# Kernel tuning notes

Measured on AMD Instinct MI355X. Metric: run time of the kernel, lower is better.

The kernel has to match this reference:

```python
import jax, jax.numpy as jnp
import numpy as np

STD = 0.01

def setup_inputs() -> dict:
    key = jax.random.key(0)
    k1, k2, k3 = jax.random.split(key, 3)
    B, T, D = 16, 4096, 512
    x = jax.random.normal(k1, (B, T, D), dtype=jnp.float32)
    att_W = jax.random.normal(k2, (D, D), dtype=jnp.float32) * STD
    att_v = jax.random.normal(k3, (D,), dtype=jnp.float32) * STD
    return {"x": x, "att_W": att_W, "att_v": att_v}

def reference(x, att_W, att_v):
    # additive attention scores: tanh(x @ W) @ v -> [B, T]
    y = jnp.tanh(jnp.einsum('btd,de->bte', x, att_W))
    scores = jnp.einsum('btd,d->bt', y, att_v)
    weights = jax.nn.softmax(scores, axis=-1)          # softmax over sequence
    out = jnp.einsum('bt,btd->bd', weights, x)         # weighted sum pooling
    return out.astype(jnp.float32)
```

## Files before the change

kernel.cpp:

```cpp
#include <hip/hip_runtime.h>
#include <hip/hip_bf16.h>
#include <math.h>

#define BB 16
#define TT 4096
#define DD 512
#define MM (BB*TT)

typedef __bf16 bf16x8 __attribute__((ext_vector_type(8)));
typedef float  f32x4  __attribute__((ext_vector_type(4)));

__device__ inline unsigned short f2bf(float f) {
    unsigned u = __builtin_bit_cast(unsigned, f) + 0x8000u;
    return (unsigned short)(u >> 16);
}

__device__ inline unsigned pack_bf16x2(float lo, float hi) {
    unsigned u0 = __builtin_bit_cast(unsigned, lo) + 0x8000u;
    unsigned u1 = __builtin_bit_cast(unsigned, hi) + 0x8000u;
    return __builtin_amdgcn_perm(u1, u0, 0x07060302);
}

__global__ void wt_kernel(const float* __restrict__ W, unsigned short* __restrict__ Wt) {
    int idx = blockIdx.x * 256 + threadIdx.x;
    int n = idx >> 9;
    int k = idx & 511;
    Wt[idx] = f2bf(W[k * DD + n]);
}

#define BM 128
#define BN 128
#define BK 64
#define LDA 72

__global__ __launch_bounds__(256) void scores_kernel(
        const float* __restrict__ x, const unsigned short* __restrict__ Wt,
        const float* __restrict__ v, float* __restrict__ spart) {
    __shared__ unsigned short As[BM * LDA];
    __shared__ unsigned short Bs[BN * LDA];
    __shared__ float sbuf[2][BM];

    const int tid  = threadIdx.x;
    const int m0   = blockIdx.x * BM;
    const int n0   = blockIdx.y * BN;
    const int wid  = tid >> 6;
    const int lane = tid & 63;
    const int wm   = wid >> 1;
    const int wn   = wid & 1;
    const int l15  = lane & 15;
    const int q    = lane >> 4;

    f32x4 acc[4][4];
    #pragma unroll
    for (int i = 0; i < 4; i++)
        #pragma unroll
        for (int j = 0; j < 4; j++)
            acc[i][j] = (f32x4){0.f, 0.f, 0.f, 0.f};

    for (int k0 = 0; k0 < DD; k0 += BK) {
        #pragma unroll
        for (int i = 0; i < 8; i++) {
            int idx = i * 256 + tid;
            int row = idx >> 4;
            int c4  = idx & 15;
            float4 f = *(const float4*)(x + (size_t)(m0 + row) * DD + k0 + c4 * 4);
            uint2 p;
            p.x = pack_bf16x2(f.x, f.y);
            p.y = pack_bf16x2(f.z, f.w);
            *(uint2*)(&As[row * LDA + c4 * 4]) = p;
        }
        #pragma unroll
        for (int i = 0; i < 4; i++) {
            int idx = i * 256 + tid;
            int row = idx >> 3;
            int c8  = idx & 7;
            uint4 u = *(const uint4*)(Wt + (size_t)(n0 + row) * DD + k0 + c8 * 8);
            *(uint4*)(&Bs[row * LDA + c8 * 8]) = u;
        }
        __syncthreads();

        #pragma unroll
        for (int s = 0; s < 2; s++) {
            const int ko = s * 32 + q * 8;
            bf16x8 a[4], b[4];
            #pragma unroll
            for (int mi = 0; mi < 4; mi++)
                a[mi] = *(const bf16x8*)(&As[(wm * 64 + mi * 16 + l15) * LDA + ko]);
            #pragma unroll
            for (int ni = 0; ni < 4; ni++)
                b[ni] = *(const bf16x8*)(&Bs[(wn * 64 + ni * 16 + l15) * LDA + ko]);
            #pragma unroll
            for (int mi = 0; mi < 4; mi++)
                #pragma unroll
                for (int ni = 0; ni < 4; ni++)
                    acc[mi][ni] = __builtin_amdgcn_mfma_f32_16x16x32_bf16(
                        a[mi], b[ni], acc[mi][ni], 0, 0, 0);
        }
        __syncthreads();
    }

    float vv[4];
    #pragma unroll
    for (int ni = 0; ni < 4; ni++)
        vv[ni] = v[n0 + wn * 64 + ni * 16 + l15];

    #pragma unroll
    for (int mi = 0; mi < 4; mi++) {
        #pragma unroll
        for (int r = 0; r < 4; r++) {
            float sum = 0.f;
            #pragma unroll
            for (int ni = 0; ni < 4; ni++)
                sum += tanhf(acc[mi][ni][r]) * vv[ni];
            sum += __shfl_xor(sum, 1);
            sum += __shfl_xor(sum, 2);
            sum += __shfl_xor(sum, 4);
            sum += __shfl_xor(sum, 8);
            if (l15 == 0)
                sbuf[wn][wm * 64 + mi * 16 + q * 4 + r] = sum;
        }
    }
    __syncthreads();
    if (tid < BM)
        spart[(size_t)blockIdx.y * MM + m0 + tid] = sbuf[0][tid] + sbuf[1][tid];
}

__global__ void softmax_kernel(const float* __restrict__ spart, float* __restrict__ weights) {
    const int b = blockIdx.x;
    const int tid = threadIdx.x;
    __shared__ float wred[4];

    float s[16];
    float mx = -1e30f;
    #pragma unroll
    for (int i = 0; i < 16; i++) {
        int t = b * TT + i * 256 + tid;
        float sv = spart[t] + spart[MM + t] + spart[2 * MM + t] + spart[3 * MM + t];
        s[i] = sv;
        mx = fmaxf(mx, sv);
    }
    #pragma unroll
    for (int off = 32; off; off >>= 1) mx = fmaxf(mx, __shfl_xor(mx, off));
    if ((tid & 63) == 0) wred[tid >> 6] = mx;
    __syncthreads();
    mx = fmaxf(fmaxf(wred[0], wred[1]), fmaxf(wred[2], wred[3]));
    __syncthreads();

    float sum = 0.f;
    #pragma unroll
    for (int i = 0; i < 16; i++) { s[i] = __expf(s[i] - mx); sum += s[i]; }
    #pragma unroll
    for (int off = 32; off; off >>= 1) sum += __shfl_xor(sum, off);
    if ((tid & 63) == 0) wred[tid >> 6] = sum;
    __syncthreads();
    sum = wred[0] + wred[1] + wred[2] + wred[3];

    const float inv = 1.0f / sum;
    #pragma unroll
    for (int i = 0; i < 16; i++)
        weights[b * TT + i * 256 + tid] = s[i] * inv;
}

#define TCH 128
__global__ void pool_kernel(const float* __restrict__ x, const float* __restrict__ weights,
                            float* __restrict__ out) {
    __shared__ float wsm[TCH];
    const int b  = blockIdx.y;
    const int t0 = blockIdx.x * TCH;
    const int tid = threadIdx.x;
    if (tid < TCH) wsm[tid] = weights[b * TT + t0 + tid];
    __syncthreads();

    float2 acc = {0.f, 0.f};
    const float* xp = x + ((size_t)b * TT + t0) * DD + tid * 2;
    #pragma unroll 4
    for (int t = 0; t < TCH; t++) {
        float2 xv = *(const float2*)(xp + (size_t)t * DD);
        float w = wsm[t];
        acc.x += w * xv.x;
        acc.y += w * xv.y;
    }
    atomicAdd(&out[b * DD + tid * 2],     acc.x);
    atomicAdd(&out[b * DD + tid * 2 + 1], acc.y);
}

extern "C" void kernel_launch(void* const* d_in, const int* in_sizes, int n_in,
                              void* d_out, int out_size, void* d_ws, size_t ws_size,
                              hipStream_t stream) {
    (void)in_sizes; (void)n_in; (void)out_size; (void)ws_size;
    const float* x = (const float*)d_in[0];
    const float* W = (const float*)d_in[1];
    const float* v = (const float*)d_in[2];
    float* out = (float*)d_out;

    unsigned short* Wt    = (unsigned short*)d_ws;
    float* spart          = (float*)((char*)d_ws + 512 * 1024);
    float* weights        = (float*)((char*)d_ws + 512 * 1024 + 1024 * 1024);

    hipMemsetAsync(d_out, 0, BB * DD * sizeof(float), stream);

    wt_kernel<<<DD * DD / 256, 256, 0, stream>>>(W, Wt);

    dim3 g1(MM / BM, DD / BN);
    scores_kernel<<<g1, 256, 0, stream>>>(x, Wt, v, spart);

    softmax_kernel<<<BB, 256, 0, stream>>>(spart, weights);

    pool_kernel<<<dim3(TT / TCH, BB), 256, 0, stream>>>(x, weights, out);
}
```

Baseline: 292.2 us.

## Pre-cast x to bf16 and stream tiles into LDS via global_load_lds

Adds a cast kernel that converts x to bf16 once into workspace. The scores GEMM then loads bf16 tiles of x and W straight into LDS with global_load_lds, using an XOR-swizzled layout instead of padding. The pooling kernel also reads the bf16 copy. This is meant to halve the bytes re-read across the four N-tile passes and the pooling pass, and to remove per-tile conversion work. In exchange it adds an extra full pass over x, needs a large workspace (with a fallback to the old fp32 path when the workspace is too small), and pools over rounded bf16 values of x.

```diff
diff --git a/kernel.cpp b/kernel.cpp
--- a/kernel.cpp
+++ b/kernel.cpp
@@ -19,6 +19,24 @@
     unsigned u0 = __builtin_bit_cast(unsigned, lo) + 0x8000u;
     unsigned u1 = __builtin_bit_cast(unsigned, hi) + 0x8000u;
     return __builtin_amdgcn_perm(u1, u0, 0x07060302);
+}
+
+__device__ inline void gld_lds16(const unsigned short* g, unsigned short* l) {
+    __builtin_amdgcn_global_load_lds(
+        (const __attribute__((address_space(1))) unsigned int*)(const void*)g,
+        (__attribute__((address_space(3))) unsigned int*)(void*)l, 16, 0, 0);
+}
+
+__global__ void cast_kernel(const float* __restrict__ x, unsigned short* __restrict__ xb) {
+    size_t i = (size_t)(blockIdx.x * 256 + threadIdx.x) * 8;
+    float4 f0 = *(const float4*)(x + i);
+    float4 f1 = *(const float4*)(x + i + 4);
+    uint4 o;
+    o.x = pack_bf16x2(f0.x, f0.y);
+    o.y = pack_bf16x2(f0.z, f0.w);
+    o.z = pack_bf16x2(f1.x, f1.y);
+    o.w = pack_bf16x2(f1.z, f1.w);
+    *(uint4*)(xb + i) = o;
 }
 
 __global__ void wt_kernel(const float* __restrict__ W, unsigned short* __restrict__ Wt) {
@@ -31,13 +49,12 @@
 #define BM 128
 #define BN 128
 #define BK 64
-#define LDA 72
-
-__global__ __launch_bounds__(256) void scores_kernel(
-        const float* __restrict__ x, const unsigned short* __restrict__ Wt,
+
+__global__ __launch_bounds__(256) void scores_bf16_kernel(
+        const unsigned short* __restrict__ xb, const unsigned short* __restrict__ Wt,
         const float* __restrict__ v, float* __restrict__ spart) {
-    __shared__ unsigned short As[BM * LDA];
-    __shared__ unsigned short Bs[BN * LDA];
+    __shared__ unsigned short As[BM * BK];
+    __shared__ unsigned short Bs[BN * BK];
     __shared__ float sbuf[2][BM];
 
     const int tid  = threadIdx.x;
@@ -50,6 +67,99 @@
     const int l15  = lane & 15;
     const int q    = lane >> 4;
 
+    int srow[4], scol[4];
+    #pragma unroll
+    for (int i = 0; i < 4; i++) {
+        int ci = (wid * 4 + i) * 64 + lane;
+        srow[i] = ci >> 3;
+        scol[i] = ((ci & 7) ^ (srow[i] & 7)) * 8;
+    }
+
+    f32x4 acc[4][4];
+    #pragma unroll
+    for (int i = 0; i < 4; i++)
+        #pragma unroll
+        for (int j = 0; j < 4; j++)
+            acc[i][j] = (f32x4){0.f, 0.f, 0.f, 0.f};
+
+    for (int k0 = 0; k0 < DD; k0 += BK) {
+        #pragma unroll
+        for (int i = 0; i < 4; i++) {
+            gld_lds16(xb + (size_t)(m0 + srow[i]) * DD + k0 + scol[i],
+                      &As[(wid * 4 + i) * 512]);
+            gld_lds16(Wt + (size_t)(n0 + srow[i]) * DD + k0 + scol[i],
+                      &Bs[(wid * 4 + i) * 512]);
+        }
+        __syncthreads();
+
+        #pragma unroll
+        for (int s = 0; s < 2; s++) {
+            const int c = s * 4 + q;
+            bf16x8 a[4], b[4];
+            #pragma unroll
+            for (int mi = 0; mi < 4; mi++) {
+                int R = wm * 64 + mi * 16 + l15;
+                a[mi] = *(const bf16x8*)(&As[R * BK + ((c ^ (R & 7)) * 8)]);
+            }
+            #pragma unroll
+            for (int ni = 0; ni < 4; ni++) {
+                int R = wn * 64 + ni * 16 + l15;
+                b[ni] = *(const bf16x8*)(&Bs[R * BK + ((c ^ (R & 7)) * 8)]);
+            }
+            #pragma unroll
+            for (int mi = 0; mi < 4; mi++)
+                #pragma unroll
+                for (int ni = 0; ni < 4; ni++)
+                    acc[mi][ni] = __builtin_amdgcn_mfma_f32_16x16x32_bf16(
+                        a[mi], b[ni], acc[mi][ni], 0, 0, 0);
+        }
+        __syncthreads();
+    }
+
+    float vv[4];
+    #pragma unroll
+    for (int ni = 0; ni < 4; ni++)
+        vv[ni] = v[n0 + wn * 64 + ni * 16 + l15];
+
+    #pragma unroll
+    for (int mi = 0; mi < 4; mi++) {
+        #pragma unroll
+        for (int r = 0; r < 4; r++) {
+            float sum = 0.f;
+            #pragma unroll
+            for (int ni = 0; ni < 4; ni++)
+                sum += tanhf(acc[mi][ni][r]) * vv[ni];
+            sum += __shfl_xor(sum, 1);
+            sum += __shfl_xor(sum, 2);
+            sum += __shfl_xor(sum, 4);
+            sum += __shfl_xor(sum, 8);
+            if (l15 == 0)
+                sbuf[wn][wm * 64 + mi * 16 + q * 4 + r] = sum;
+        }
+    }
+    __syncthreads();
+    if (tid < BM)
+        spart[(size_t)blockIdx.y * MM + m0 + tid] = sbuf[0][tid] + sbuf[1][tid];
+}
+
+#define LDA 72
+__global__ __launch_bounds__(256) void scores_f32_kernel(
+        const float* __restrict__ x, const unsigned short* __restrict__ Wt,
+        const float* __restrict__ v, float* __restrict__ spart) {
+    __shared__ unsigned short As[BM * LDA];
+    __shared__ unsigned short Bs[BN * LDA];
+    __shared__ float sbuf[2][BM];
+
+    const int tid  = threadIdx.x;
+    const int m0   = blockIdx.x * BM;
+    const int n0   = blockIdx.y * BN;
+    const int wid  = tid >> 6;
+    const int lane = tid & 63;
+    const int wm   = wid >> 1;
+    const int wn   = wid & 1;
+    const int l15  = lane & 15;
+    const int q    = lane >> 4;
+
     f32x4 acc[4][4];
     #pragma unroll
     for (int i = 0; i < 4; i++)
@@ -162,8 +272,32 @@
 }
 
 #define TCH 128
-__global__ void pool_kernel(const float* __restrict__ x, const float* __restrict__ weights,
-                            float* __restrict__ out) {
+__global__ void pool_bf16_kernel(const unsigned short* __restrict__ xb,
+                                 const float* __restrict__ weights, float* __restrict__ out) {
+    __shared__ float wsm[TCH];
+    const int b  = blockIdx.y;
+    const int t0 = blockIdx.x * TCH;
+    const int tid = threadIdx.x;
+    if (tid < TCH) wsm[tid] = weights[b * TT + t0 + tid];
+    __syncthreads();
+
+    float2 acc = {0.f, 0.f};
+    const unsigned short* xp = xb + ((size_t)b * TT + t0) * DD + tid * 2;
+    #pragma unroll 4
+    for (int t = 0; t < TCH; t++) {
+        unsigned u = *(const unsigned*)(xp + (size_t)t * DD);
+        float lo = __builtin_bit_cast(float, u << 16);
+        float hi = __builtin_bit_cast(float, u & 0xFFFF0000u);
+        float w = wsm[t];
+        acc.x += w * lo;
+        acc.y += w * hi;
+    }
+    atomicAdd(&out[b * DD + tid * 2],     acc.x);
+    atomicAdd(&out[b * DD + tid * 2 + 1], acc.y);
+}
+
+__global__ void pool_f32_kernel(const float* __restrict__ x, const float* __restrict__ weights,
+                                float* __restrict__ out) {
     __shared__ float wsm[TCH];
     const int b  = blockIdx.y;
     const int t0 = blockIdx.x * TCH;
@@ -187,24 +321,39 @@
 extern "C" void kernel_launch(void* const* d_in, const int* in_sizes, int n_in,
                               void* d_out, int out_size, void* d_ws, size_t ws_size,
                               hipStream_t stream) {
-    (void)in_sizes; (void)n_in; (void)out_size; (void)ws_size;
+    (void)in_sizes; (void)n_in; (void)out_size;
     const float* x = (const float*)d_in[0];
     const float* W = (const float*)d_in[1];
     const float* v = (const float*)d_in[2];
     float* out = (float*)d_out;
 
-    unsigned short* Wt    = (unsigned short*)d_ws;
-    float* spart          = (float*)((char*)d_ws + 512 * 1024);
-    float* weights        = (float*)((char*)d_ws + 512 * 1024 + 1024 * 1024);
+    const size_t XB_BYTES = (size_t)MM * DD * 2;
+    const size_t NEED = XB_BYTES + 512*1024 + 1024*1024 + 256*1024;
 
     hipMemsetAsync(d_out, 0, BB * DD * sizeof(float), stream);
 
-    wt_kernel<<<DD * DD / 256, 256, 0, stream>>>(W, Wt);
-
-    dim3 g1(MM / BM, DD / BN);
-    scores_kernel<<<g1, 256, 0, stream>>>(x, Wt, v, spart);
-
-    softmax_kernel<<<BB, 256, 0, stream>>>(spart, weights);
-
-    pool_kernel<<<dim3(TT / TCH, BB), 256, 0, stream>>>(x, weights, out);
-}
+    if (ws_size >= NEED) {
+        unsigned short* xb   = (unsigned short*)d_ws;
+        unsigned short* Wt   = (unsigned short*)((char*)d_ws + XB_BYTES);
+        float* spart         = (float*)((char*)d_ws + XB_BYTES + 512*1024);
+        float* weights       = (float*)((char*)d_ws + XB_BYTES + 512*1024 + 1024*1024);
+
+        wt_kernel<<<DD * DD / 256, 256, 0, stream>>>(W, Wt);
+        cast_kernel<<<(size_t)MM * DD / 8 / 256, 256, 0, stream>>>(x, xb);
+
+        dim3 g1(MM / BM, DD / BN);
+        scores_bf16_kernel<<<g1, 256, 0, stream>>>(xb, Wt, v, spart);
+        softmax_kernel<<<BB, 256, 0, stream>>>(spart, weights);
+        pool_bf16_kernel<<<dim3(TT / TCH, BB), 256, 0, stream>>>(xb, weights, out);
+    } else {
+        unsigned short* Wt   = (unsigned short*)d_ws;
+        float* spart         = (float*)((char*)d_ws + 512*1024);
+        float* weights       = (float*)((char*)d_ws + 512*1024 + 1024*1024);
+
+        wt_kernel<<<DD * DD / 256, 256, 0, stream>>>(W, Wt);
+        dim3 g1(MM / BM, DD / BN);
+        scores_f32_kernel<<<g1, 256, 0, stream>>>(x, Wt, v, spart);
+        softmax_kernel<<<BB, 256, 0, stream>>>(spart, weights);
+        pool_f32_kernel<<<dim3(TT / TCH, BB), 256, 0, stream>>>(x, weights, out);
+    }
+}
```

Result: no change. 289.4 us (-1.0%).

## Restructure scores GEMM to hold full-K row tile in LDS, stream W from global

Applied to the files above, without the earlier changes.

The scores kernel now loads a 64-row slab of x (all 512 columns, as bf16 with an XOR swizzle) into LDS once. Each wave then covers 128 output columns, reading W fragments directly from global/L2 through register double/triple buffering. This removes the four-way N split, the repeated x reads and conversions across column blocks, the per-K-step barriers and the partial-score buffer. tanhf is also replaced with an exp/rcp approximation. Costs are 64KB of LDS per block, which limits occupancy, and W traffic served from L2 by every block.

```diff
diff --git a/kernel.cpp b/kernel.cpp
--- a/kernel.cpp
+++ b/kernel.cpp
@@ -19,6 +19,11 @@
     unsigned u0 = __builtin_bit_cast(unsigned, lo) + 0x8000u;
     unsigned u1 = __builtin_bit_cast(unsigned, hi) + 0x8000u;
     return __builtin_amdgcn_perm(u1, u0, 0x07060302);
+}
+
+__device__ inline float tanh_fast(float y) {
+    float e = __expf(2.0f * y);
+    return 1.0f - 2.0f * __builtin_amdgcn_rcpf(e + 1.0f);
 }
 
 __global__ void wt_kernel(const float* __restrict__ W, unsigned short* __restrict__ Wt) {
@@ -28,104 +33,123 @@
     Wt[idx] = f2bf(W[k * DD + n]);
 }
 
-#define BM 128
-#define BN 128
-#define BK 64
-#define LDA 72
-
-__global__ __launch_bounds__(256) void scores_kernel(
+__global__ __launch_bounds__(256, 2) void scores_kernel(
         const float* __restrict__ x, const unsigned short* __restrict__ Wt,
-        const float* __restrict__ v, float* __restrict__ spart) {
-    __shared__ unsigned short As[BM * LDA];
-    __shared__ unsigned short Bs[BN * LDA];
-    __shared__ float sbuf[2][BM];
+        const float* __restrict__ v, float* __restrict__ scores) {
+    __shared__ unsigned short As[64 * DD];
+    __shared__ float sbuf[4][64];
 
     const int tid  = threadIdx.x;
-    const int m0   = blockIdx.x * BM;
-    const int n0   = blockIdx.y * BN;
+    const int m0   = blockIdx.x * 64;
     const int wid  = tid >> 6;
     const int lane = tid & 63;
-    const int wm   = wid >> 1;
-    const int wn   = wid & 1;
     const int l15  = lane & 15;
     const int q    = lane >> 4;
-
-    f32x4 acc[4][4];
-    #pragma unroll
-    for (int i = 0; i < 4; i++)
-        #pragma unroll
-        for (int j = 0; j < 4; j++)
-            acc[i][j] = (f32x4){0.f, 0.f, 0.f, 0.f};
-
-    for (int k0 = 0; k0 < DD; k0 += BK) {
-        #pragma unroll
-        for (int i = 0; i < 8; i++) {
-            int idx = i * 256 + tid;
-            int row = idx >> 4;
-            int c4  = idx & 15;
-            float4 f = *(const float4*)(x + (size_t)(m0 + row) * DD + k0 + c4 * 4);
-            uint2 p;
-            p.x = pack_bf16x2(f.x, f.y);
-            p.y = pack_bf16x2(f.z, f.w);
-            *(uint2*)(&As[row * LDA + c4 * 4]) = p;
+    const int r3   = l15 & 7;
+
+    #pragma unroll
+    for (int i = 0; i < 16; i++) {
+        int u = i * 256 + tid;
+        int r = u >> 6;
+        int c = u & 63;
+        const float* gp = x + (size_t)(m0 + r) * DD + c * 8;
+        float4 f0 = *(const float4*)(gp);
+        float4 f1 = *(const float4*)(gp + 4);
+        uint4 o;
+        o.x = pack_bf16x2(f0.x, f0.y);
+        o.y = pack_bf16x2(f0.z, f0.w);
+        o.z = pack_bf16x2(f1.x, f1.y);
+        o.w = pack_bf16x2(f1.z, f1.w);
+        *(uint4*)(&As[r * DD + (c ^ (r & 7)) * 8]) = o;
+    }
+    __syncthreads();
+
+    float vpart[4][4];
+    #pragma unroll
+    for (int mi = 0; mi < 4; mi++)
+        #pragma unroll
+        for (int rr = 0; rr < 4; rr++)
+            vpart[mi][rr] = 0.f;
+
+    #define A_FRAG(mi, s) (*(const bf16x8*)(&As[((mi)*16 + l15) * DD + ((((s)*4 + q) ^ r3) * 8)]))
+
+    #pragma unroll
+    for (int p = 0; p < 2; p++) {
+        const int n0 = wid * 128 + p * 64;
+
+        const unsigned short* bp[4];
+        #pragma unroll
+        for (int ni = 0; ni < 4; ni++)
+            bp[ni] = Wt + (size_t)(n0 + ni * 16 + l15) * DD + q * 8;
+
+        f32x4 acc[4][4];
+        #pragma unroll
+        for (int mi = 0; mi < 4; mi++)
+            #pragma unroll
+            for (int ni = 0; ni < 4; ni++)
+                acc[mi][ni] = (f32x4){0.f, 0.f, 0.f, 0.f};
+
+        bf16x8 a[2][4], b[3][4];
+        #pragma unroll
+        for (int mi = 0; mi < 4; mi++) a[0][mi] = A_FRAG(mi, 0);
+        #pragma unroll
+        for (int ni = 0; ni < 4; ni++) {
+            b[0][ni] = *(const bf16x8*)(bp[ni]);
+            b[1][ni] = *(const bf16x8*)(bp[ni] + 32);
         }
-        #pragma unroll
-        for (int i = 0; i < 4; i++) {
-            int idx = i * 256 + tid;
-            int row = idx >> 3;
-            int c8  = idx & 7;
-            uint4 u = *(const uint4*)(Wt + (size_t)(n0 + row) * DD + k0 + c8 * 8);
-            *(uint4*)(&Bs[row * LDA + c8 * 8]) = u;
-        }
-        __syncthreads();
-
-        #pragma unroll
-        for (int s = 0; s < 2; s++) {
-            const int ko = s * 32 + q * 8;
-            bf16x8 a[4], b[4];
+
+        #pragma unroll
+        for (int s = 0; s < 16; s++) {
+            const int cur = s & 1;
+            if (s < 15) {
+                #pragma unroll
+                for (int mi = 0; mi < 4; mi++) a[cur ^ 1][mi] = A_FRAG(mi, s + 1);
+            }
+            if (s < 14) {
+                #pragma unroll
+                for (int ni = 0; ni < 4; ni++)
+                    b[(s + 2) % 3][ni] = *(const bf16x8*)(bp[ni] + (s + 2) * 32);
+            }
             #pragma unroll
             for (int mi = 0; mi < 4; mi++)
-                a[mi] = *(const bf16x8*)(&As[(wm * 64 + mi * 16 + l15) * LDA + ko]);
+                #pragma unroll
+                for (int ni = 0; ni < 4; ni++)
+                    acc[mi][ni] = __builtin_amdgcn_mfma_f32_16x16x32_bf16(
+                        a[cur][mi], b[s % 3][ni], acc[mi][ni], 0, 0, 0);
+        }
+
+        float vv[4];
+        #pragma unroll
+        for (int ni = 0; ni < 4; ni++)
+            vv[ni] = v[n0 + ni * 16 + l15];
+        #pragma unroll
+        for (int mi = 0; mi < 4; mi++)
             #pragma unroll
             for (int ni = 0; ni < 4; ni++)
-                b[ni] = *(const bf16x8*)(&Bs[(wn * 64 + ni * 16 + l15) * LDA + ko]);
-            #pragma unroll
-            for (int mi = 0; mi < 4; mi++)
-                #pragma unroll
-                for (int ni = 0; ni < 4; ni++)
-                    acc[mi][ni] = __builtin_amdgcn_mfma_f32_16x16x32_bf16(
-                        a[mi], b[ni], acc[mi][ni], 0, 0, 0);
-        }
-        __syncthreads();
-    }
-
-    float vv[4];
-    #pragma unroll
-    for (int ni = 0; ni < 4; ni++)
-        vv[ni] = v[n0 + wn * 64 + ni * 16 + l15];
-
-    #pragma unroll
-    for (int mi = 0; mi < 4; mi++) {
-        #pragma unroll
-        for (int r = 0; r < 4; r++) {
-            float sum = 0.f;
-            #pragma unroll
-            for (int ni = 0; ni < 4; ni++)
-                sum += tanhf(acc[mi][ni][r]) * vv[ni];
+                #pragma unroll
+                for (int rr = 0; rr < 4; rr++)
+                    vpart[mi][rr] += tanh_fast(acc[mi][ni][rr]) * vv[ni];
+    }
+    #undef A_FRAG
+
+    #pragma unroll
+    for (int mi = 0; mi < 4; mi++)
+        #pragma unroll
+        for (int rr = 0; rr < 4; rr++) {
+            float sum = vpart[mi][rr];
             sum += __shfl_xor(sum, 1);
             sum += __shfl_xor(sum, 2);
             sum += __shfl_xor(sum, 4);
             sum += __shfl_xor(sum, 8);
             if (l15 == 0)
-                sbuf[wn][wm * 64 + mi * 16 + q * 4 + r] = sum;
+                sbuf[wid][mi * 16 + q * 4 + rr] = sum;
         }
-    }
-    __syncthreads();
-    if (tid < BM)
-        spart[(size_t)blockIdx.y * MM + m0 + tid] = sbuf[0][tid] + sbuf[1][tid];
-}
-
-__global__ void softmax_kernel(const float* __restrict__ spart, float* __restrict__ weights) {
+    __syncthreads();
+    if (tid < 64)
+        scores[m0 + tid] = sbuf[0][tid] + sbuf[1][tid] + sbuf[2][tid] + sbuf[3][tid];
+}
+
+__global__ void softmax_kernel(const float* __restrict__ scores, float* __restrict__ weights) {
     const int b = blockIdx.x;
     const int tid = threadIdx.x;
     __shared__ float wred[4];
@@ -134,8 +158,7 @@
     float mx = -1e30f;
     #pragma unroll
     for (int i = 0; i < 16; i++) {
-        int t = b * TT + i * 256 + tid;
-        float sv = spart[t] + spart[MM + t] + spart[2 * MM + t] + spart[3 * MM + t];
+        float sv = scores[b * TT + i * 256 + tid];
         s[i] = sv;
         mx = fmaxf(mx, sv);
     }
@@ -193,18 +216,17 @@
     const float* v = (const float*)d_in[2];
     float* out = (float*)d_out;
 
-    unsigned short* Wt    = (unsigned short*)d_ws;
-    float* spart          = (float*)((char*)d_ws + 512 * 1024);
-    float* weights        = (float*)((char*)d_ws + 512 * 1024 + 1024 * 1024);
+    unsigned short* Wt = (unsigned short*)d_ws;
+    float* scores      = (float*)((char*)d_ws + 512 * 1024);
+    float* weights     = (float*)((char*)d_ws + 512 * 1024 + 256 * 1024);
 
     hipMemsetAsync(d_out, 0, BB * DD * sizeof(float), stream);
 
     wt_kernel<<<DD * DD / 256, 256, 0, stream>>>(W, Wt);
 
-    dim3 g1(MM / BM, DD / BN);
-    scores_kernel<<<g1, 256, 0, stream>>>(x, Wt, v, spart);
-
-    softmax_kernel<<<BB, 256, 0, stream>>>(spart, weights);
+    scores_kernel<<<MM / 64, 256, 0, stream>>>(x, Wt, v, scores);
+
+    softmax_kernel<<<BB, 256, 0, stream>>>(scores, weights);
 
     pool_kernel<<<dim3(TT / TCH, BB), 256, 0, stream>>>(x, weights, out);
 }
```

Result: no change. 288.5 us (-1.3%).
